# Kernel optimization log

Measured on AMD Instinct MI355X. Metric: run time of the kernel, lower is better.

The kernel has to match this reference:

```python
import jax, jax.numpy as jnp
import numpy as np

EMB = 1024
HEADS = 16
HEAD_SIZE = EMB // HEADS


def setup_inputs() -> dict:
    key = jax.random.key(0)
    ks = jax.random.split(key, 10)
    B, L = 2, 2048
    s = 1.0 / np.sqrt(EMB)
    inp = {
        "x": jax.random.normal(ks[0], (B, L, EMB), jnp.float32),
        "ln_g": jnp.ones((EMB,), jnp.float32),
        "ln_b": jnp.zeros((EMB,), jnp.float32),
        "Wq": jax.random.normal(ks[1], (EMB, EMB), jnp.float32) * s,
        "bq": jnp.zeros((EMB,), jnp.float32),
        "Wk": jax.random.normal(ks[2], (EMB, EMB), jnp.float32) * s,
        "bk": jnp.zeros((EMB,), jnp.float32),
        "Wv": jax.random.normal(ks[3], (EMB, EMB), jnp.float32) * s,
        "bv": jnp.zeros((EMB,), jnp.float32),
        "Wo": jax.random.normal(ks[4], (EMB, EMB), jnp.float32) * s,
        "bo": jnp.zeros((EMB,), jnp.float32),
    }
    return inp


def _attn_block(x, ln_g, ln_b, Wq, bq, Wk, bk, Wv, bv, Wo, bo):
    B, L, D = x.shape
    # LayerNorm (eps=1e-5 as torch default)
    mu = jnp.mean(x, axis=-1, keepdims=True)
    var = jnp.mean(jnp.square(x - mu), axis=-1, keepdims=True)
    h = (x - mu) * jax.lax.rsqrt(var + 1e-5) * ln_g + ln_b
    # QKV projections (torch Linear: x @ W.T + b), split heads -> [B,H,L,hs]
    def heads(y):
        return y.reshape(B, L, HEADS, HEAD_SIZE).transpose(0, 2, 1, 3)
    q = heads(h @ Wq.T + bq)
    k = heads(h @ Wk.T + bk)
    v = heads(h @ Wv.T + bv)
    # scaled dot-product attention (no mask; dropout = identity in eval)
    scores = jnp.einsum("bhqd,bhkd->bhqk", q, k) * (HEAD_SIZE ** -0.5)
    w = jax.nn.softmax(scores, axis=-1)
    o = jnp.einsum("bhqk,bhkd->bhqd", w, v)
    o = o.transpose(0, 2, 1, 3).reshape(B, L, D)
    return o @ Wo.T + bo


def reference(x, ln_g, ln_b, Wq, bq, Wk, bk, Wv, bv, Wo, bo):
    return _attn_block(x, ln_g, ln_b, Wq, bq, Wk, bk, Wv, bv, Wo, bo)
```

## Files before the change

kernel.cpp:

```cpp
#include <hip/hip_runtime.h>
#include <stdint.h>

#define EMB 1024
#define SEQL 2048
#define HEADS 16
#define HS 64

typedef __attribute__((ext_vector_type(8))) short bfx8;
typedef __attribute__((ext_vector_type(4))) float f32x4;
typedef __attribute__((ext_vector_type(16))) float f32x16;
typedef __attribute__((ext_vector_type(4))) unsigned short us4;

__device__ __forceinline__ unsigned short f2bf(float f) {
  union { float f; unsigned u; } x; x.f = f;
  unsigned r = x.u + 0x7fffu + ((x.u >> 16) & 1u);
  return (unsigned short)(r >> 16);
}

__device__ __forceinline__ unsigned cvtpk(float lo, float hi) {
  unsigned r;
  asm("v_cvt_pk_bf16_f32 %0, %1, %2" : "=v"(r) : "v"(lo), "v"(hi));
  return r;
}

__device__ __forceinline__ float expv(float x) {
  float r;
  asm("v_exp_f32 %0, %1" : "=v"(r) : "v"(x));
  return r;
}

__device__ __forceinline__ float max3f(float a, float b, float c) {
  float r;
  asm("v_max3_f32 %0, %1, %2, %3" : "=v"(r) : "v"(a), "v"(b), "v"(c));
  return r;
}

__device__ __forceinline__ void gll16(const void* g, void* l) {
  __builtin_amdgcn_global_load_lds(
      (const __attribute__((address_space(1))) unsigned int*)g,
      (__attribute__((address_space(3))) unsigned int*)l, 16, 0, 0);
}

__global__ __launch_bounds__(256) void ln_kernel(
    const float* __restrict__ x, const float* __restrict__ gam,
    const float* __restrict__ bet, unsigned short* __restrict__ h) {
  const int row = blockIdx.x;
  const int tid = threadIdx.x;
  const float4 v = reinterpret_cast<const float4*>(x + (size_t)row * EMB)[tid];
  float s = v.x + v.y + v.z + v.w;
  float sq = v.x * v.x + v.y * v.y + v.z * v.z + v.w * v.w;
  #pragma unroll
  for (int m = 1; m < 64; m <<= 1) {
    s += __shfl_xor(s, m, 64);
    sq += __shfl_xor(sq, m, 64);
  }
  __shared__ float red[8];
  const int lane = tid & 63, wave = tid >> 6;
  if (lane == 0) { red[wave] = s; red[wave + 4] = sq; }
  __syncthreads();
  s = red[0] + red[1] + red[2] + red[3];
  sq = red[4] + red[5] + red[6] + red[7];
  const float mu = s * (1.0f / EMB);
  const float var = sq * (1.0f / EMB) - mu * mu;
  const float rs = rsqrtf(var + 1e-5f);
  const float4 gg = reinterpret_cast<const float4*>(gam)[tid];
  const float4 bb = reinterpret_cast<const float4*>(bet)[tid];
  us4 o;
  o.x = f2bf((v.x - mu) * rs * gg.x + bb.x);
  o.y = f2bf((v.y - mu) * rs * gg.y + bb.y);
  o.z = f2bf((v.z - mu) * rs * gg.z + bb.z);
  o.w = f2bf((v.w - mu) * rs * gg.w + bb.w);
  reinterpret_cast<us4*>(h + (size_t)row * EMB)[tid] = o;
}

__global__ __launch_bounds__(256) void cvt_kernel(
    const float* __restrict__ s0, const float* __restrict__ s1,
    const float* __restrict__ s2, const float* __restrict__ s3,
    unsigned short* __restrict__ d) {
  const int m = blockIdx.x >> 10;
  const int blk = blockIdx.x & 1023;
  const float* s = (m == 0) ? s0 : (m == 1) ? s1 : (m == 2) ? s2 : s3;
  unsigned short* dd = d + (size_t)m * EMB * EMB;
  const int idx = blk * 256 + threadIdx.x;
  const float4 v = reinterpret_cast<const float4*>(s)[idx];
  us4 o;
  o.x = f2bf(v.x); o.y = f2bf(v.y); o.z = f2bf(v.z); o.w = f2bf(v.w);
  reinterpret_cast<us4*>(dd)[idx] = o;
}

__device__ __forceinline__ void gemm_tile(
    const unsigned short* __restrict__ Ag, const unsigned short* __restrict__ Bg,
    int m0, int n0, int K, char* lA, char* lB, f32x4 acc[4][4]) {
  const int tid = threadIdx.x;
  const int lane = tid & 63, wave = tid >> 6;
  const int g = lane >> 4, c = lane & 15;
  const int wr = wave >> 1, wc = wave & 1;

  const f32x4 zero = {0.f, 0.f, 0.f, 0.f};
  #pragma unroll
  for (int i = 0; i < 4; ++i)
    #pragma unroll
    for (int j = 0; j < 4; ++j) acc[i][j] = zero;

  const int Dbase = (wave * 4 * 64 + lane) * 16;
  for (int k0 = 0; k0 < K; k0 += 64) {
    __syncthreads();
    #pragma unroll
    for (int i = 0; i < 4; ++i) {
      const int Db = Dbase + i * 1024;
      const int row = Db >> 7;
      const int col = ((Db & 127) ^ ((row & 7) << 4)) >> 1;
      gll16(Ag + (size_t)(m0 + row) * K + (k0 + col), lA + (wave * 4 + i) * 1024);
      gll16(Bg + (size_t)(n0 + row) * K + (k0 + col), lB + (wave * 4 + i) * 1024);
    }
    __syncthreads();
    #pragma unroll
    for (int kf = 0; kf < 2; ++kf) {
      bfx8 af[4], bfr[4];
      #pragma unroll
      for (int i = 0; i < 4; ++i) {
        const int ra = wr * 64 + i * 16 + c;
        af[i] = *(const bfx8*)(lA + ra * 128 + ((kf * 64 + g * 16) ^ ((ra & 7) << 4)));
        const int rb = wc * 64 + i * 16 + c;
        bfr[i] = *(const bfx8*)(lB + rb * 128 + ((kf * 64 + g * 16) ^ ((rb & 7) << 4)));
      }
      #pragma unroll
      for (int i = 0; i < 4; ++i)
        #pragma unroll
        for (int j = 0; j < 4; ++j)
          acc[i][j] = __builtin_amdgcn_mfma_f32_16x16x32_bf16(af[i], bfr[j], acc[i][j], 0, 0, 0);
    }
  }
}

__global__ __launch_bounds__(256, 3) void qkv_gemm(
    const unsigned short* __restrict__ h, const unsigned short* __restrict__ wbf,
    const float* __restrict__ bq, const float* __restrict__ bk,
    const float* __restrict__ bv, unsigned short* __restrict__ qb,
    unsigned short* __restrict__ kb, unsigned short* __restrict__ vtb) {
  __shared__ char lA[16384];
  __shared__ char lB[16384];
  f32x4 acc[4][4];
  const int m0 = blockIdx.x * 128;
  const int n0g = blockIdx.y * 128;
  const int mat = n0g >> 10;
  const int n0 = n0g & 1023;
  gemm_tile(h, wbf + (size_t)mat * EMB * EMB, m0, n0, EMB, lA, lB, acc);

  const float* bias = (mat == 0) ? bq : (mat == 1) ? bk : bv;
  const int lane = threadIdx.x & 63, wave = threadIdx.x >> 6;
  const int g = lane >> 4, c = lane & 15;
  const int wr = wave >> 1, wc = wave & 1;
  #pragma unroll
  for (int i = 0; i < 4; ++i) {
    #pragma unroll
    for (int j = 0; j < 4; ++j) {
      const int col = n0 + wc * 64 + j * 16 + c;
      const float bz = bias[col];
      const int hh = col >> 6, d = col & 63;
      #pragma unroll
      for (int r = 0; r < 4; ++r) {
        const int row = m0 + wr * 64 + i * 16 + 4 * g + r;
        const int bidx = row >> 11, l = row & 2047;
        const unsigned short bv16 = f2bf(acc[i][j][r] + bz);
        if (mat < 2) {
          unsigned short* dst = (mat == 0) ? qb : kb;
          dst[(((size_t)(bidx * HEADS + hh) * SEQL + l) << 6) + d] = bv16;
        } else {
          vtb[((size_t)(bidx * HEADS + hh) * HS + d) * SEQL + l] = bv16;
        }
      }
    }
  }
}

__global__ __launch_bounds__(256, 2) void attn_kernel(
    const unsigned short* __restrict__ qb, const unsigned short* __restrict__ kb,
    const unsigned short* __restrict__ vtb, unsigned short* __restrict__ ob) {
  __shared__ char lK[4][8192];
  __shared__ char lV[4][8192];
  const int tid = threadIdx.x, lane = tid & 63, wave = tid >> 6;
  const int l31 = lane & 31, hi = lane >> 5;
  const int sw = (l31 & 7) << 4;
  const int qblk = blockIdx.x;
  const int bh = blockIdx.y;
  const unsigned short* qp = qb + (size_t)bh * SEQL * HS;
  const unsigned short* kp = kb + (size_t)bh * SEQL * HS;
  const unsigned short* vp = vtb + (size_t)bh * HS * SEQL;
  const int qbase = qblk * 128 + wave * 32;

  bfx8 aq[4];
  #pragma unroll
  for (int kf = 0; kf < 4; ++kf)
    aq[kf] = *(const bfx8*)(qp + (size_t)(qbase + l31) * HS + kf * 16 + hi * 8);

  const float SCL = 0.125f * 1.44269504089f;
  const float THR = 11.5416f;
  const bfx8 vone = {0x3F80, 0x3F80, 0x3F80, 0x3F80, 0x3F80, 0x3F80, 0x3F80, 0x3F80};

  float mst = -INFINITY;
  f32x16 oacc0, oacc1, lacc;
  const f32x16 zero16 = {0.f,0.f,0.f,0.f,0.f,0.f,0.f,0.f,0.f,0.f,0.f,0.f,0.f,0.f,0.f,0.f};
  oacc0 = zero16; oacc1 = zero16; lacc = zero16;

  const int sbase = wave * 2048;
  const int Db0 = sbase + lane * 16, Db1 = Db0 + 1024;
  const int sr0 = Db0 >> 7, sr1 = Db1 >> 7;
  const int sc0 = ((Db0 & 127) ^ ((sr0 & 7) << 4)) >> 1;
  const int sc1 = ((Db1 & 127) ^ ((sr1 & 7) << 4)) >> 1;
  const unsigned short* k0s = kp + (size_t)sr0 * HS + sc0;
  const unsigned short* k1s = kp + (size_t)sr1 * HS + sc1;
  const unsigned short* v0s = vp + (size_t)sr0 * SEQL + sc0;
  const unsigned short* v1s = vp + (size_t)sr1 * SEQL + sc1;

  gll16(k0s, lK[0] + sbase); gll16(k1s, lK[0] + sbase + 1024);
  gll16(v0s, lV[0] + sbase); gll16(v1s, lV[0] + sbase + 1024);
  gll16(k0s + 64 * HS, lK[1] + sbase); gll16(k1s + 64 * HS, lK[1] + sbase + 1024);
  gll16(v0s + 64, lV[1] + sbase); gll16(v1s + 64, lV[1] + sbase + 1024);

  const unsigned short* kf0 = k0s + 2 * 64 * HS;
  const unsigned short* kf1 = k1s + 2 * 64 * HS;
  const unsigned short* vf0 = v0s + 2 * 64;
  const unsigned short* vf1 = v1s + 2 * 64;

  auto step = [&](const char* lKc, const char* lVc, char* nK, char* nV,
                  const int wait, const bool doStage) {
    if (doStage) {
      gll16(kf0, nK + sbase); gll16(kf1, nK + sbase + 1024);
      gll16(vf0, nV + sbase); gll16(vf1, nV + sbase + 1024);
      kf0 += 64 * HS; kf1 += 64 * HS; vf0 += 64; vf1 += 64;
    }
    if (wait == 8)      asm volatile("s_waitcnt vmcnt(8)" ::: "memory");
    else if (wait == 4) asm volatile("s_waitcnt vmcnt(4)" ::: "memory");
    else                asm volatile("s_waitcnt vmcnt(0)" ::: "memory");
    __builtin_amdgcn_s_barrier();
    __builtin_amdgcn_sched_barrier(0);

    f32x16 sa = zero16, sb = zero16;
    __builtin_amdgcn_s_setprio(1);
    #pragma unroll
    for (int kf = 0; kf < 4; ++kf) {
      const int ko = (32 * kf + 16 * hi) ^ sw;
      const bfx8 a0 = *(const bfx8*)(lKc + l31 * 128 + ko);
      const bfx8 a1 = *(const bfx8*)(lKc + l31 * 128 + 4096 + ko);
      sa = __builtin_amdgcn_mfma_f32_32x32x16_bf16(a0, aq[kf], sa, 0, 0, 0);
      sb = __builtin_amdgcn_mfma_f32_32x32x16_bf16(a1, aq[kf], sb, 0, 0, 0);
    }
    __builtin_amdgcn_s_setprio(0);

    float m0 = max3f(sa[0], sa[1], sa[2]);
    float m1 = max3f(sa[3], sa[4], sa[5]);
    float m2 = max3f(sa[6], sa[7], sa[8]);
    float m3 = max3f(sa[9], sa[10], sa[11]);
    float m4 = max3f(sa[12], sa[13], sa[14]);
    float n0 = max3f(sb[0], sb[1], sb[2]);
    float n1 = max3f(sb[3], sb[4], sb[5]);
    float n2 = max3f(sb[6], sb[7], sb[8]);
    float n3 = max3f(sb[9], sb[10], sb[11]);
    float n4 = max3f(sb[12], sb[13], sb[14]);
    m0 = max3f(m0, m1, m2);
    m3 = max3f(m3, m4, sa[15]);
    n0 = max3f(n0, n1, n2);
    n3 = max3f(n3, n4, sb[15]);
    const float sm = fmaxf(fmaxf(m0, m3), fmaxf(n0, n3));

    if (__any(sm * SCL > mst + THR)) {
      float mt = sm * SCL;
      mt = fmaxf(mt, __shfl_xor(mt, 32, 64));
      const float mn = fmaxf(mst, mt);
      const float al = exp2f(mst - mn);
      mst = mn;
      #pragma unroll
      for (int r = 0; r < 16; ++r) {
        const int qi = (r & 3) + 8 * (r >> 2) + 4 * hi;
        const float alq = __shfl(al, qi, 64);
        lacc[r] *= alq;
        oacc0[r] *= alq;
        oacc1[r] *= alq;
      }
    }

    #pragma unroll
    for (int r = 0; r < 16; ++r) {
      sa[r] = expv(fmaf(sa[r], SCL, -mst));
      sb[r] = expv(fmaf(sb[r], SCL, -mst));
    }

    __builtin_amdgcn_s_setprio(1);
    #pragma unroll
    for (int kf = 0; kf < 4; ++kf) {
      const int bb = 8 * (kf & 1);
      float p0, p1, p2, p3, p4, p5, p6, p7;
      if (kf < 2) {
        p0 = sa[bb + 0]; p1 = sa[bb + 1]; p2 = sa[bb + 2]; p3 = sa[bb + 3];
        p4 = sa[bb + 4]; p5 = sa[bb + 5]; p6 = sa[bb + 6]; p7 = sa[bb + 7];
      } else {
        p0 = sb[bb + 0]; p1 = sb[bb + 1]; p2 = sb[bb + 2]; p3 = sb[bb + 3];
        p4 = sb[bb + 4]; p5 = sb[bb + 5]; p6 = sb[bb + 6]; p7 = sb[bb + 7];
      }
      unsigned w0 = cvtpk(p0, p1), w2 = cvtpk(p4, p5);
      unsigned w1 = cvtpk(p2, p3), w3 = cvtpk(p6, p7);
      asm("v_permlane32_swap_b32 %0, %1" : "+v"(w0), "+v"(w2));
      asm("v_permlane32_swap_b32 %0, %1" : "+v"(w1), "+v"(w3));
      union { unsigned u[4]; bfx8 v; } pa;
      pa.u[0] = w0; pa.u[1] = w1; pa.u[2] = w2; pa.u[3] = w3;
      lacc = __builtin_amdgcn_mfma_f32_32x32x16_bf16(pa.v, vone, lacc, 0, 0, 0);
      const int vo = (32 * kf + 16 * hi) ^ sw;
      const bfx8 b0 = *(const bfx8*)(lVc + l31 * 128 + vo);
      const bfx8 b1 = *(const bfx8*)(lVc + l31 * 128 + 4096 + vo);
      oacc0 = __builtin_amdgcn_mfma_f32_32x32x16_bf16(pa.v, b0, oacc0, 0, 0, 0);
      oacc1 = __builtin_amdgcn_mfma_f32_32x32x16_bf16(pa.v, b1, oacc1, 0, 0, 0);
    }
    __builtin_amdgcn_s_setprio(0);
  };

  for (int t = 0; t < 28; t += 4) {
    step(lK[0], lV[0], lK[2], lV[2], 8, true);
    step(lK[1], lV[1], lK[3], lV[3], 8, true);
    step(lK[2], lV[2], lK[0], lV[0], 8, true);
    step(lK[3], lV[3], lK[1], lV[1], 8, true);
  }
  step(lK[0], lV[0], lK[2], lV[2], 8, true);
  step(lK[1], lV[1], lK[3], lV[3], 8, true);
  step(lK[2], lV[2], lK[0], lV[0], 4, false);
  step(lK[3], lV[3], lK[1], lV[1], 0, false);

  const int b = bh >> 4, hh = bh & 15;
  #pragma unroll
  for (int r = 0; r < 16; ++r) {
    const float inv = 1.f / lacc[r];
    const int row = qbase + (r & 3) + 8 * (r >> 2) + 4 * hi;
    unsigned short* orow = ob + (size_t)(b * SEQL + row) * EMB + hh * 64;
    orow[l31] = f2bf(oacc0[r] * inv);
    orow[32 + l31] = f2bf(oacc1[r] * inv);
  }
}

__global__ __launch_bounds__(256, 2) void out_gemm(
    const unsigned short* __restrict__ ob, const unsigned short* __restrict__ wo,
    const float* __restrict__ bo, float* __restrict__ out) {
  __shared__ char lA[16384];
  __shared__ char lB[16384];
  f32x4 acc[4][4];
  const int m0 = blockIdx.x * 128;
  const int n0 = blockIdx.y * 128;
  gemm_tile(ob, wo, m0, n0, EMB, lA, lB, acc);

  const int lane = threadIdx.x & 63, wave = threadIdx.x >> 6;
  const int g = lane >> 4, c = lane & 15;
  const int wr = wave >> 1, wc = wave & 1;
  #pragma unroll
  for (int i = 0; i < 4; ++i)
    #pragma unroll
    for (int j = 0; j < 4; ++j) {
      const int col = n0 + wc * 64 + j * 16 + c;
      const float bz = bo[col];
      #pragma unroll
      for (int r = 0; r < 4; ++r) {
        const int row = m0 + wr * 64 + i * 16 + 4 * g + r;
        out[(size_t)row * EMB + col] = acc[i][j][r] + bz;
      }
    }
}

extern "C" void kernel_launch(void* const* d_in, const int* in_sizes, int n_in,
                              void* d_out, int out_size, void* d_ws, size_t ws_size,
                              hipStream_t stream) {
  const float* x   = (const float*)d_in[0];
  const float* lng = (const float*)d_in[1];
  const float* lnb = (const float*)d_in[2];
  const float* Wq  = (const float*)d_in[3];
  const float* bq  = (const float*)d_in[4];
  const float* Wk  = (const float*)d_in[5];
  const float* bk  = (const float*)d_in[6];
  const float* Wv  = (const float*)d_in[7];
  const float* bv  = (const float*)d_in[8];
  const float* Wo  = (const float*)d_in[9];
  const float* bo  = (const float*)d_in[10];

  char* ws = (char*)d_ws;
  unsigned short* h   = (unsigned short*)(ws);
  unsigned short* wbf = (unsigned short*)(ws + 8388608);
  unsigned short* qb  = (unsigned short*)(ws + 16777216);
  unsigned short* kb  = (unsigned short*)(ws + 25165824);
  unsigned short* vtb = (unsigned short*)(ws + 33554432);
  unsigned short* ob  = (unsigned short*)(ws + 41943040);
  float* out = (float*)d_out;

  ln_kernel<<<dim3(4096), dim3(256), 0, stream>>>(x, lng, lnb, h);
  cvt_kernel<<<dim3(4096), dim3(256), 0, stream>>>(Wq, Wk, Wv, Wo, wbf);
  qkv_gemm<<<dim3(32, 24), dim3(256), 0, stream>>>(h, wbf, bq, bk, bv, qb, kb, vtb);
  attn_kernel<<<dim3(16, 32), dim3(256), 0, stream>>>(qb, kb, vtb, ob);
  out_gemm<<<dim3(32, 8), dim3(256), 0, stream>>>(ob, wbf + (size_t)3 * EMB * EMB, bo, out);
}
```

Measured before the change: 123.9 us.

## Merge LayerNorm and weight-cast kernels; split attention step into two 32-key halves

Combines the LayerNorm kernel and the fp32-to-bf16 weight conversion into one launch with 8192 blocks, branching on block index, so one kernel launch and its gap go away. The attention inner step now handles the 64-key tile as two 32-key halves. Each half computes its scores, updates the running max and rescales, then exponentiates and feeds P·V. This lowers live score registers and interleaves softmax with MFMA work, but it adds an extra max-check and possible rescale per half.

```diff
diff --git a/kernel.cpp b/kernel.cpp
--- a/kernel.cpp
+++ b/kernel.cpp
@@ -41,51 +41,52 @@
       (__attribute__((address_space(3))) unsigned int*)l, 16, 0, 0);
 }
 
-__global__ __launch_bounds__(256) void ln_kernel(
+__global__ __launch_bounds__(256) void lncvt_kernel(
     const float* __restrict__ x, const float* __restrict__ gam,
-    const float* __restrict__ bet, unsigned short* __restrict__ h) {
-  const int row = blockIdx.x;
-  const int tid = threadIdx.x;
-  const float4 v = reinterpret_cast<const float4*>(x + (size_t)row * EMB)[tid];
-  float s = v.x + v.y + v.z + v.w;
-  float sq = v.x * v.x + v.y * v.y + v.z * v.z + v.w * v.w;
-  #pragma unroll
-  for (int m = 1; m < 64; m <<= 1) {
-    s += __shfl_xor(s, m, 64);
-    sq += __shfl_xor(sq, m, 64);
-  }
-  __shared__ float red[8];
-  const int lane = tid & 63, wave = tid >> 6;
-  if (lane == 0) { red[wave] = s; red[wave + 4] = sq; }
-  __syncthreads();
-  s = red[0] + red[1] + red[2] + red[3];
-  sq = red[4] + red[5] + red[6] + red[7];
-  const float mu = s * (1.0f / EMB);
-  const float var = sq * (1.0f / EMB) - mu * mu;
-  const float rs = rsqrtf(var + 1e-5f);
-  const float4 gg = reinterpret_cast<const float4*>(gam)[tid];
-  const float4 bb = reinterpret_cast<const float4*>(bet)[tid];
-  us4 o;
-  o.x = f2bf((v.x - mu) * rs * gg.x + bb.x);
-  o.y = f2bf((v.y - mu) * rs * gg.y + bb.y);
-  o.z = f2bf((v.z - mu) * rs * gg.z + bb.z);
-  o.w = f2bf((v.w - mu) * rs * gg.w + bb.w);
-  reinterpret_cast<us4*>(h + (size_t)row * EMB)[tid] = o;
-}
-
-__global__ __launch_bounds__(256) void cvt_kernel(
+    const float* __restrict__ bet, unsigned short* __restrict__ h,
     const float* __restrict__ s0, const float* __restrict__ s1,
     const float* __restrict__ s2, const float* __restrict__ s3,
     unsigned short* __restrict__ d) {
-  const int m = blockIdx.x >> 10;
-  const int blk = blockIdx.x & 1023;
-  const float* s = (m == 0) ? s0 : (m == 1) ? s1 : (m == 2) ? s2 : s3;
-  unsigned short* dd = d + (size_t)m * EMB * EMB;
-  const int idx = blk * 256 + threadIdx.x;
-  const float4 v = reinterpret_cast<const float4*>(s)[idx];
-  us4 o;
-  o.x = f2bf(v.x); o.y = f2bf(v.y); o.z = f2bf(v.z); o.w = f2bf(v.w);
-  reinterpret_cast<us4*>(dd)[idx] = o;
+  const int tid = threadIdx.x;
+  if (blockIdx.x < 4096) {
+    const int row = blockIdx.x;
+    const float4 v = reinterpret_cast<const float4*>(x + (size_t)row * EMB)[tid];
+    float s = v.x + v.y + v.z + v.w;
+    float sq = v.x * v.x + v.y * v.y + v.z * v.z + v.w * v.w;
+    #pragma unroll
+    for (int m = 1; m < 64; m <<= 1) {
+      s += __shfl_xor(s, m, 64);
+      sq += __shfl_xor(sq, m, 64);
+    }
+    __shared__ float red[8];
+    const int lane = tid & 63, wave = tid >> 6;
+    if (lane == 0) { red[wave] = s; red[wave + 4] = sq; }
+    __syncthreads();
+    s = red[0] + red[1] + red[2] + red[3];
+    sq = red[4] + red[5] + red[6] + red[7];
+    const float mu = s * (1.0f / EMB);
+    const float var = sq * (1.0f / EMB) - mu * mu;
+    const float rs = rsqrtf(var + 1e-5f);
+    const float4 gg = reinterpret_cast<const float4*>(gam)[tid];
+    const float4 bb = reinterpret_cast<const float4*>(bet)[tid];
+    us4 o;
+    o.x = f2bf((v.x - mu) * rs * gg.x + bb.x);
+    o.y = f2bf((v.y - mu) * rs * gg.y + bb.y);
+    o.z = f2bf((v.z - mu) * rs * gg.z + bb.z);
+    o.w = f2bf((v.w - mu) * rs * gg.w + bb.w);
+    reinterpret_cast<us4*>(h + (size_t)row * EMB)[tid] = o;
+  } else {
+    const int bid = blockIdx.x - 4096;
+    const int m = bid >> 10;
+    const int blk = bid & 1023;
+    const float* s = (m == 0) ? s0 : (m == 1) ? s1 : (m == 2) ? s2 : s3;
+    unsigned short* dd = d + (size_t)m * EMB * EMB;
+    const int idx = blk * 256 + tid;
+    const float4 v = reinterpret_cast<const float4*>(s)[idx];
+    us4 o;
+    o.x = f2bf(v.x); o.y = f2bf(v.y); o.z = f2bf(v.z); o.w = f2bf(v.w);
+    reinterpret_cast<us4*>(dd)[idx] = o;
+  }
 }
 
 __device__ __forceinline__ void gemm_tile(
@@ -223,46 +224,29 @@
   const unsigned short* vf0 = v0s + 2 * 64;
   const unsigned short* vf1 = v1s + 2 * 64;
 
-  auto step = [&](const char* lKc, const char* lVc, char* nK, char* nV,
-                  const int wait, const bool doStage) {
-    if (doStage) {
-      gll16(kf0, nK + sbase); gll16(kf1, nK + sbase + 1024);
-      gll16(vf0, nV + sbase); gll16(vf1, nV + sbase + 1024);
-      kf0 += 64 * HS; kf1 += 64 * HS; vf0 += 64; vf1 += 64;
-    }
-    if (wait == 8)      asm volatile("s_waitcnt vmcnt(8)" ::: "memory");
-    else if (wait == 4) asm volatile("s_waitcnt vmcnt(4)" ::: "memory");
-    else                asm volatile("s_waitcnt vmcnt(0)" ::: "memory");
-    __builtin_amdgcn_s_barrier();
-    __builtin_amdgcn_sched_barrier(0);
-
-    f32x16 sa = zero16, sb = zero16;
+  auto proc_half = [&](const char* kptr, const char* lVc, const int kfv) {
+    f32x16 s;
     __builtin_amdgcn_s_setprio(1);
-    #pragma unroll
-    for (int kf = 0; kf < 4; ++kf) {
+    {
+      const bfx8 a0 = *(const bfx8*)(kptr + l31 * 128 + ((16 * hi) ^ sw));
+      s = __builtin_amdgcn_mfma_f32_32x32x16_bf16(a0, aq[0], zero16, 0, 0, 0);
+    }
+    #pragma unroll
+    for (int kf = 1; kf < 4; ++kf) {
       const int ko = (32 * kf + 16 * hi) ^ sw;
-      const bfx8 a0 = *(const bfx8*)(lKc + l31 * 128 + ko);
-      const bfx8 a1 = *(const bfx8*)(lKc + l31 * 128 + 4096 + ko);
-      sa = __builtin_amdgcn_mfma_f32_32x32x16_bf16(a0, aq[kf], sa, 0, 0, 0);
-      sb = __builtin_amdgcn_mfma_f32_32x32x16_bf16(a1, aq[kf], sb, 0, 0, 0);
+      const bfx8 a0 = *(const bfx8*)(kptr + l31 * 128 + ko);
+      s = __builtin_amdgcn_mfma_f32_32x32x16_bf16(a0, aq[kf], s, 0, 0, 0);
     }
     __builtin_amdgcn_s_setprio(0);
 
-    float m0 = max3f(sa[0], sa[1], sa[2]);
-    float m1 = max3f(sa[3], sa[4], sa[5]);
-    float m2 = max3f(sa[6], sa[7], sa[8]);
-    float m3 = max3f(sa[9], sa[10], sa[11]);
-    float m4 = max3f(sa[12], sa[13], sa[14]);
-    float n0 = max3f(sb[0], sb[1], sb[2]);
-    float n1 = max3f(sb[3], sb[4], sb[5]);
-    float n2 = max3f(sb[6], sb[7], sb[8]);
-    float n3 = max3f(sb[9], sb[10], sb[11]);
-    float n4 = max3f(sb[12], sb[13], sb[14]);
+    float m0 = max3f(s[0], s[1], s[2]);
+    float m1 = max3f(s[3], s[4], s[5]);
+    float m2 = max3f(s[6], s[7], s[8]);
+    float m3 = max3f(s[9], s[10], s[11]);
+    float m4 = max3f(s[12], s[13], s[14]);
     m0 = max3f(m0, m1, m2);
-    m3 = max3f(m3, m4, sa[15]);
-    n0 = max3f(n0, n1, n2);
-    n3 = max3f(n3, n4, sb[15]);
-    const float sm = fmaxf(fmaxf(m0, m3), fmaxf(n0, n3));
+    m3 = max3f(m3, m4, s[15]);
+    const float sm = fmaxf(m0, m3);
 
     if (__any(sm * SCL > mst + THR)) {
       float mt = sm * SCL;
@@ -281,37 +265,42 @@
     }
 
     #pragma unroll
-    for (int r = 0; r < 16; ++r) {
-      sa[r] = expv(fmaf(sa[r], SCL, -mst));
-      sb[r] = expv(fmaf(sb[r], SCL, -mst));
-    }
+    for (int r = 0; r < 16; ++r) s[r] = expv(fmaf(s[r], SCL, -mst));
 
     __builtin_amdgcn_s_setprio(1);
     #pragma unroll
-    for (int kf = 0; kf < 4; ++kf) {
-      const int bb = 8 * (kf & 1);
-      float p0, p1, p2, p3, p4, p5, p6, p7;
-      if (kf < 2) {
-        p0 = sa[bb + 0]; p1 = sa[bb + 1]; p2 = sa[bb + 2]; p3 = sa[bb + 3];
-        p4 = sa[bb + 4]; p5 = sa[bb + 5]; p6 = sa[bb + 6]; p7 = sa[bb + 7];
-      } else {
-        p0 = sb[bb + 0]; p1 = sb[bb + 1]; p2 = sb[bb + 2]; p3 = sb[bb + 3];
-        p4 = sb[bb + 4]; p5 = sb[bb + 5]; p6 = sb[bb + 6]; p7 = sb[bb + 7];
-      }
-      unsigned w0 = cvtpk(p0, p1), w2 = cvtpk(p4, p5);
-      unsigned w1 = cvtpk(p2, p3), w3 = cvtpk(p6, p7);
+    for (int h2 = 0; h2 < 2; ++h2) {
+      const int bb = 8 * h2;
+      unsigned w0 = cvtpk(s[bb + 0], s[bb + 1]), w2 = cvtpk(s[bb + 4], s[bb + 5]);
+      unsigned w1 = cvtpk(s[bb + 2], s[bb + 3]), w3 = cvtpk(s[bb + 6], s[bb + 7]);
       asm("v_permlane32_swap_b32 %0, %1" : "+v"(w0), "+v"(w2));
       asm("v_permlane32_swap_b32 %0, %1" : "+v"(w1), "+v"(w3));
       union { unsigned u[4]; bfx8 v; } pa;
       pa.u[0] = w0; pa.u[1] = w1; pa.u[2] = w2; pa.u[3] = w3;
       lacc = __builtin_amdgcn_mfma_f32_32x32x16_bf16(pa.v, vone, lacc, 0, 0, 0);
-      const int vo = (32 * kf + 16 * hi) ^ sw;
+      const int vo = (32 * (kfv + h2) + 16 * hi) ^ sw;
       const bfx8 b0 = *(const bfx8*)(lVc + l31 * 128 + vo);
       const bfx8 b1 = *(const bfx8*)(lVc + l31 * 128 + 4096 + vo);
       oacc0 = __builtin_amdgcn_mfma_f32_32x32x16_bf16(pa.v, b0, oacc0, 0, 0, 0);
       oacc1 = __builtin_amdgcn_mfma_f32_32x32x16_bf16(pa.v, b1, oacc1, 0, 0, 0);
     }
     __builtin_amdgcn_s_setprio(0);
+  };
+
+  auto step = [&](const char* lKc, const char* lVc, char* nK, char* nV,
+                  const int wait, const bool doStage) {
+    if (doStage) {
+      gll16(kf0, nK + sbase); gll16(kf1, nK + sbase + 1024);
+      gll16(vf0, nV + sbase); gll16(vf1, nV + sbase + 1024);
+      kf0 += 64 * HS; kf1 += 64 * HS; vf0 += 64; vf1 += 64;
+    }
+    if (wait == 8)      asm volatile("s_waitcnt vmcnt(8)" ::: "memory");
+    else if (wait == 4) asm volatile("s_waitcnt vmcnt(4)" ::: "memory");
+    else                asm volatile("s_waitcnt vmcnt(0)" ::: "memory");
+    __builtin_amdgcn_s_barrier();
+    __builtin_amdgcn_sched_barrier(0);
+    proc_half(lKc,        lVc, 0);
+    proc_half(lKc + 4096, lVc, 2);
   };
 
   for (int t = 0; t < 28; t += 4) {
@@ -387,8 +376,8 @@
   unsigned short* ob  = (unsigned short*)(ws + 41943040);
   float* out = (float*)d_out;
 
-  ln_kernel<<<dim3(4096), dim3(256), 0, stream>>>(x, lng, lnb, h);
-  cvt_kernel<<<dim3(4096), dim3(256), 0, stream>>>(Wq, Wk, Wv, Wo, wbf);
+  lncvt_kernel<<<dim3(8192), dim3(256), 0, stream>>>(x, lng, lnb, h,
+                                                     Wq, Wk, Wv, Wo, wbf);
   qkv_gemm<<<dim3(32, 24), dim3(256), 0, stream>>>(h, wbf, bq, bk, bv, qb, kb, vtb);
   attn_kernel<<<dim3(16, 32), dim3(256), 0, stream>>>(qb, kb, vtb, ob);
   out_gemm<<<dim3(32, 8), dim3(256), 0, stream>>>(ob, wbf + (size_t)3 * EMB * EMB, bo, out);
```

New measurement: 123.8 us. About the same (-0.1%).
